# Kernel tuning notes

Measured on AMD Instinct MI355X. Metric: run time of the kernel, lower is better.

Reference implementation:

```python
import jax, jax.numpy as jnp
import numpy as np

N_NODES = 100000
N_EDGES = 1600000
DIMS = [2, 16, 32, 32, 32, 32, 32, 16, 2]


def setup_inputs() -> dict:
    key = jax.random.key(0)
    ks = jax.random.split(key, 20)
    inp = {}
    inp["x"] = jax.random.normal(ks[0], (N_NODES, DIMS[0]), dtype=jnp.float32)
    inp["edge_index"] = jax.random.randint(ks[1], (2, N_EDGES), 0, N_NODES, dtype=jnp.int64)
    for i in range(8):
        fan_in, fan_out = DIMS[i], DIMS[i + 1]
        scale = 1.0 / np.sqrt(fan_in)
        inp[f"W{i+1}"] = jax.random.uniform(ks[2 + i], (fan_in, fan_out), minval=-scale, maxval=scale, dtype=jnp.float32)
        inp[f"b{i+1}"] = jnp.zeros((fan_out,), dtype=jnp.float32)
    return inp


def _gcn_layer(h, W, b, src, dst, norm, n):
    # GCNConv: h' = D^{-1/2} (A+I) D^{-1/2} (h W) + b
    m = (h @ W)[src] * norm[:, None]          # [E+N, d_out] gathered messages
    return jax.ops.segment_sum(m, dst, num_segments=n) + b


def reference(x, edge_index, W1, b1, W2, b2, W3, b3, W4, b4, W5, b5, W6, b6, W7, b7, W8, b8):
    n = x.shape[0]
    x_orig = x[:, :2]
    loops = jnp.arange(n, dtype=edge_index.dtype)
    src = jnp.concatenate([edge_index[0], loops])  # self-loops appended
    dst = jnp.concatenate([edge_index[1], loops])
    deg = jax.ops.segment_sum(jnp.ones(src.shape[0], x.dtype), dst, num_segments=n)
    dinv = jnp.where(deg > 0, jax.lax.rsqrt(deg), 0.0)
    norm = dinv[src] * dinv[dst]               # symmetric normalization per edge
    params = [(W1, b1), (W2, b2), (W3, b3), (W4, b4), (W5, b5), (W6, b6), (W7, b7), (W8, b8)]
    h = x
    for i, (W, b) in enumerate(params):
        h = _gcn_layer(h, W, b, src, dst, norm, n)
        if i < 7:
            h = jax.nn.relu(h)  # dropout is identity in eval mode
    return h + x_orig
```

## Files before the change

### kernel.cpp

```cpp
#include <hip/hip_runtime.h>
#include <hip/hip_fp16.h>

#define NN 100000
#define NE 1600000
#define SCAN_BLK 1024
#define NBLK ((NN + SCAN_BLK - 1) / SCAN_BLK)

#define EB 3072
#define NBE ((NE + EB - 1) / EB)
#define BSH 10
#define NBUCK ((NN + 1023) >> BSH)
#define BCAP 18432


__global__ void k_init(int* __restrict__ bcur) {
    int i = blockIdx.x * blockDim.x + threadIdx.x;
    if (i < NBUCK) bcur[i] = i * BCAP;
}

__global__ __launch_bounds__(256) void k_bucket(
    const int* __restrict__ ei, int* __restrict__ bcur,
    long long* __restrict__ pairs, int nE) {
    __shared__ int cnt[NBUCK];
    __shared__ int sc[NBUCK];
    __shared__ int rc[NBUCK];
    __shared__ int gbase[NBUCK];
    __shared__ int tmp[256];
    __shared__ long long st[EB];

    int base = blockIdx.x * EB;
    int lim = nE - base; if (lim > EB) lim = EB;
    int tid = threadIdx.x;

    for (int i = tid; i < NBUCK; i += 256) cnt[i] = 0;
    __syncthreads();
    for (int i = tid; i < lim; i += 256) {
        int d = ei[nE + base + i];
        atomicAdd(&cnt[d >> BSH], 1);
    }
    __syncthreads();
    {
        int v = (tid < NBUCK) ? cnt[tid] : 0;
        tmp[tid] = v;
        __syncthreads();
        for (int off = 1; off < 256; off <<= 1) {
            int add = (tid >= off) ? tmp[tid - off] : 0;
            __syncthreads();
            tmp[tid] += add;
            __syncthreads();
        }
        if (tid < NBUCK) {
            int e = tmp[tid] - v;
            sc[tid] = e;
            rc[tid] = e;
            gbase[tid] = (v > 0) ? atomicAdd(&bcur[tid], v) : 0;
        }
    }
    __syncthreads();
    for (int i = tid; i < lim; i += 256) {
        int s = ei[base + i];
        int d = ei[nE + base + i];
        int p = atomicAdd(&rc[d >> BSH], 1);
        st[p] = ((long long)d << 32) | (unsigned int)s;
    }
    __syncthreads();
    for (int i = tid; i < lim; i += 256) {
        long long pr = st[i];
        int b = (int)(pr >> 32) >> BSH;
        pairs[gbase[b] + (i - sc[b])] = pr;
    }
}

__global__ __launch_bounds__(256) void k_count2(
    const long long* __restrict__ pairs, const int* __restrict__ bcur,
    int* __restrict__ deg) {
    __shared__ int cnt[1 << BSH];
    int b = blockIdx.x;
    int gb = b * BCAP;
    int m = bcur[b] - gb;
    for (int i = threadIdx.x; i < (1 << BSH); i += 256) cnt[i] = 0;
    __syncthreads();
    for (int i = threadIdx.x; i < m; i += 256) {
        int d = (int)(pairs[gb + i] >> 32);
        atomicAdd(&cnt[d & ((1 << BSH) - 1)], 1);
    }
    __syncthreads();
    int base = b << BSH;
    for (int i = threadIdx.x; i < (1 << BSH); i += 256) {
        int v = base + i;
        if (v < NN) deg[v] = cnt[i];
    }
}

__global__ __launch_bounds__(SCAN_BLK) void k_scan1(
    const int* __restrict__ deg, int* __restrict__ exc, int* __restrict__ bsum, int n) {
    __shared__ int sh[SCAN_BLK];
    int tid = threadIdx.x;
    int i = blockIdx.x * SCAN_BLK + tid;
    int v = (i < n) ? ((deg[i] + 7) & ~7) : 0;
    sh[tid] = v;
    __syncthreads();
    for (int off = 1; off < SCAN_BLK; off <<= 1) {
        int add = (tid >= off) ? sh[tid - off] : 0;
        __syncthreads();
        sh[tid] += add;
        __syncthreads();
    }
    if (i < n) exc[i] = sh[tid] - v;
    if (tid == SCAN_BLK - 1) bsum[blockIdx.x] = sh[tid];
}

__global__ __launch_bounds__(128) void k_scan2(int* __restrict__ bsum, int nb) {
    __shared__ int sh[128];
    int tid = threadIdx.x;
    int v = (tid < nb) ? bsum[tid] : 0;
    sh[tid] = v;
    __syncthreads();
    for (int off = 1; off < 128; off <<= 1) {
        int add = (tid >= off) ? sh[tid - off] : 0;
        __syncthreads();
        sh[tid] += add;
        __syncthreads();
    }
    if (tid < nb) bsum[tid] = sh[tid] - v;
}

__global__ __launch_bounds__(SCAN_BLK) void k_scan3(
    const int* __restrict__ exc, const int* __restrict__ bsum,
    const int* __restrict__ deg, const float* __restrict__ x,
    int* __restrict__ rowptr, float* __restrict__ dinv,
    __half2* __restrict__ hd0, int n) {
    int i = blockIdx.x * SCAN_BLK + threadIdx.x;
    if (i >= n) return;
    int r = exc[i] + bsum[blockIdx.x];
    rowptr[i] = r;
    float dv = rsqrtf((float)(deg[i] + 1));
    dinv[i] = dv;
    hd0[i] = __floats2half2_rn(x[2 * i] * dv, x[2 * i + 1] * dv);
    if (i == n - 1) rowptr[n] = r + ((deg[i] + 7) & ~7);
    if (i == 0) hd0[n] = __floats2half2_rn(0.f, 0.f);
}

__global__ __launch_bounds__(256) void k_fill3(
    const long long* __restrict__ pairs, const int* __restrict__ bcur,
    const int* __restrict__ rowptr, int* __restrict__ csr_src) {
    __shared__ int lcur[1 << BSH];
    int b = blockIdx.x;
    int gb = b * BCAP;
    int m = bcur[b] - gb;
    int base = b << BSH;
    for (int i = threadIdx.x; i < (1 << BSH); i += 256) {
        int v = base + i;
        lcur[i] = (v < NN) ? rowptr[v] : 0;
    }
    __syncthreads();
    for (int i = threadIdx.x; i < m; i += 256) {
        long long pr = pairs[gb + i];
        int d = (int)(pr >> 32);
        int s = (int)(pr & 0xffffffffLL);
        int pos = atomicAdd(&lcur[d & ((1 << BSH) - 1)], 1);
        csr_src[pos] = s;
    }
    __syncthreads();
    for (int i = threadIdx.x; i < (1 << BSH); i += 256) {
        int v = base + i;
        if (v < NN) {
            int e = lcur[i];
            int pe = rowptr[v + 1];
            for (; e < pe; ++e) csr_src[e] = NN;
        }
    }
}


__global__ __launch_bounds__(256) void k_layer1(
    const int* __restrict__ rowptr, const int* __restrict__ csr_src,
    const __half2* __restrict__ hd0, const float* __restrict__ Wg,
    const float* __restrict__ bg, const float* __restrict__ dinv,
    __half* __restrict__ hd1, int n) {
    __shared__ float sW[32];
    if (threadIdx.x < 32) sW[threadIdx.x] = Wg[threadIdx.x];
    __syncthreads();
    int v = blockIdx.x * 16 + threadIdx.x / 16;
    int l = threadIdx.x & 15;
    if (v > n) return;
    if (v == n) { hd1[v * 16 + l] = __float2half(0.f); return; }
    int lo = rowptr[v], hi = rowptr[v + 1];
    float a0 = 0.f, a1 = 0.f;
    for (int j = lo + l; j < hi; j += 16) {
        float2 h = __half22float2(hd0[csr_src[j]]);
        a0 += h.x; a1 += h.y;
    }
#pragma unroll
    for (int off = 8; off >= 1; off >>= 1) {
        a0 += __shfl_xor(a0, off, 16);
        a1 += __shfl_xor(a1, off, 16);
    }
    float dv = dinv[v];
    float2 hs = __half22float2(hd0[v]);
    a0 = (a0 + hs.x) * dv;
    a1 = (a1 + hs.y) * dv;
    float o = bg[l] + a0 * sW[l] + a1 * sW[16 + l];
    hd1[v * 16 + l] = __float2half(fmaxf(o, 0.f) * dv);
}

template <int DIN, int DOUT, bool RELU, bool LAST, bool TWOWAY>
__global__ __launch_bounds__(256) void k_layer(
    const int* __restrict__ rowptr, const int* __restrict__ csr_src,
    const __half* __restrict__ hd_in, const float* __restrict__ Wg,
    const float* __restrict__ bg, const float* __restrict__ dinv,
    const float* __restrict__ xorig, __half* __restrict__ hout_h,
    float* __restrict__ hout_f, int n) {
    constexpr int OPL = (DOUT + DIN - 1) / DIN;
    constexpr int LPG = DIN * (TWOWAY ? 2 : 1);
    __shared__ float sW[DIN * DOUT];
    for (int i = threadIdx.x; i < DIN * DOUT; i += 256) sW[i] = Wg[i];
    __syncthreads();
    const int gpb = 256 / LPG;
    int v = blockIdx.x * gpb + (int)threadIdx.x / LPG;
    int f = threadIdx.x % DIN;
    int way = (threadIdx.x % LPG) / DIN;
    if (v > n) return;
    if (v == n) {
        if (!LAST && way == 0) {
#pragma unroll
            for (int k = 0; k < OPL; ++k) {
                int g = f + k * DIN;
                if (g < DOUT) hout_h[v * DOUT + g] = __float2half(0.f);
            }
        }
        return;
    }
    int lo = rowptr[v], hi = rowptr[v + 1];
    if (TWOWAY) {
        int nch = (hi - lo) >> 3;
        int mid = lo + (((nch + 1) >> 1) << 3);
        if (way == 0) hi = mid; else lo = mid;
    }
    float acc = 0.f;
    for (int j = lo; j < hi; j += 8) {
        int s0 = csr_src[j + 0], s1 = csr_src[j + 1], s2 = csr_src[j + 2], s3 = csr_src[j + 3];
        int s4 = csr_src[j + 4], s5 = csr_src[j + 5], s6 = csr_src[j + 6], s7 = csr_src[j + 7];
        float v0 = __half2float(hd_in[s0 * DIN + f]);
        float v1 = __half2float(hd_in[s1 * DIN + f]);
        float v2 = __half2float(hd_in[s2 * DIN + f]);
        float v3 = __half2float(hd_in[s3 * DIN + f]);
        float v4 = __half2float(hd_in[s4 * DIN + f]);
        float v5 = __half2float(hd_in[s5 * DIN + f]);
        float v6 = __half2float(hd_in[s6 * DIN + f]);
        float v7 = __half2float(hd_in[s7 * DIN + f]);
        acc += ((v0 + v1) + (v2 + v3)) + ((v4 + v5) + (v6 + v7));
    }
    if (TWOWAY) acc += __shfl_xor(acc, DIN, 64);
    float dv = dinv[v];
    float aggv = (acc + __half2float(hd_in[v * DIN + f])) * dv;

    if (TWOWAY) {
        int g = f % DOUT;
        float o = (way == 0) ? bg[g] : 0.f;
        int f2b = way * (DIN / 2);
#pragma unroll
        for (int k = 0; k < DIN / 2; ++k) {
            int f2 = f2b + k;
            o = fmaf(__shfl(aggv, f2, DIN), sW[f2 * DOUT + g], o);
        }
        o += __shfl_xor(o, DIN, 64);
        if (way == 0 && f < DOUT) {
            float r = o;
            if (RELU) r = fmaxf(r, 0.f);
            if (LAST) hout_f[v * DOUT + g] = r + xorig[v * 2 + g];
            else      hout_h[v * DOUT + g] = __float2half(r * dv);
        }
    } else {
        float o[OPL];
#pragma unroll
        for (int k = 0; k < OPL; ++k) {
            int g = f + k * DIN;
            o[k] = (g < DOUT) ? bg[g] : 0.f;
        }
#pragma unroll
        for (int f2 = 0; f2 < DIN; ++f2) {
            float hf = __shfl(aggv, f2, DIN);
#pragma unroll
            for (int k = 0; k < OPL; ++k) {
                int g = f + k * DIN;
                if (g < DOUT) o[k] = fmaf(hf, sW[f2 * DOUT + g], o[k]);
            }
        }
#pragma unroll
        for (int k = 0; k < OPL; ++k) {
            int g = f + k * DIN;
            if (g < DOUT) {
                float r = o[k];
                if (RELU) r = fmaxf(r, 0.f);
                if (LAST) hout_f[v * DOUT + g] = r + xorig[v * 2 + g];
                else      hout_h[v * DOUT + g] = __float2half(r * dv);
            }
        }
    }
}


extern "C" void kernel_launch(void* const* d_in, const int* in_sizes, int n_in,
                              void* d_out, int out_size, void* d_ws, size_t ws_size,
                              hipStream_t stream) {
    const float* x = (const float*)d_in[0];
    const int* ei = (const int*)d_in[1];
    const float* W[8];
    const float* B[8];
    for (int i = 0; i < 8; ++i) {
        W[i] = (const float*)d_in[2 + 2 * i];
        B[i] = (const float*)d_in[3 + 2 * i];
    }
    float* out = (float*)d_out;

    char* ws = (char*)d_ws;
    int*       deg     = (int*)      (ws + 0);
    float*     dinv    = (float*)    (ws + 400128);
    int*       rowptr  = (int*)      (ws + 800256);
    int*       exc     = (int*)      (ws + 1200384);
    int*       bsum    = (int*)      (ws + 1600512);
    int*       bcur    = (int*)      (ws + 1601024);
    long long* pairs   = (long long*)(ws + 1601536);
    int*       csr_src = (int*)      (ws + 16052224);
    __half*    hdA     = (__half*)   (ws + 25652224);
    __half*    hdB     = (__half*)   (ws + 32052352);

    dim3 blk(256);

    k_init<<<1, 128, 0, stream>>>(bcur);
    k_bucket<<<NBE, blk, 0, stream>>>(ei, bcur, pairs, NE);
    k_count2<<<NBUCK, blk, 0, stream>>>(pairs, bcur, deg);
    k_scan1<<<NBLK, SCAN_BLK, 0, stream>>>(deg, exc, bsum, NN);
    k_scan2<<<1, 128, 0, stream>>>(bsum, NBLK);
    k_scan3<<<NBLK, SCAN_BLK, 0, stream>>>(exc, bsum, deg, x, rowptr, dinv, (__half2*)hdA, NN);
    k_fill3<<<NBUCK, blk, 0, stream>>>(pairs, bcur, rowptr, csr_src);

    int g16 = (NN + 16) / 16;
    int gT  = (NN + 4) / 4;

    k_layer1<<<g16, blk, 0, stream>>>(rowptr, csr_src, (const __half2*)hdA, W[0], B[0], dinv, hdB, NN);
    k_layer<16, 32, true, false, false><<<g16, blk, 0, stream>>>(rowptr, csr_src, hdB, W[1], B[1], dinv, x, hdA, out, NN);
    k_layer<32, 32, true, false, true><<<gT, blk, 0, stream>>>(rowptr, csr_src, hdA, W[2], B[2], dinv, x, hdB, out, NN);
    k_layer<32, 32, true, false, true><<<gT, blk, 0, stream>>>(rowptr, csr_src, hdB, W[3], B[3], dinv, x, hdA, out, NN);
    k_layer<32, 32, true, false, true><<<gT, blk, 0, stream>>>(rowptr, csr_src, hdA, W[4], B[4], dinv, x, hdB, out, NN);
    k_layer<32, 32, true, false, true><<<gT, blk, 0, stream>>>(rowptr, csr_src, hdB, W[5], B[5], dinv, x, hdA, out, NN);
    k_layer<32, 16, true, false, true><<<gT, blk, 0, stream>>>(rowptr, csr_src, hdA, W[6], B[6], dinv, x, hdB, out, NN);
    k_layer<16, 2, false, true, false><<<g16, blk, 0, stream>>>(rowptr, csr_src, hdB, W[7], B[7], dinv, x, hdA, out, NN);
}
```

Baseline: 395.1 us.

## Map one node per wavefront with scalar neighbor indices in GCN layers

Rewrites the per-layer aggregation kernel so that each 64-lane wavefront processes a single node. The rowptr bounds and neighbor indices become wave-uniform via readfirstlane, so they can be loaded through scalar loads. Each layer shape gets its own specialized mini-matmul that splits the input features across lanes and reduces with shuffles. The intent is to cut redundant vector index loads and per-lane address math. In exchange, lanes are wasted for narrow layers (DIN=16, each gathered feature read by multiple lanes) and parallelism per node is lower. The edge-bucketing block size is also doubled.

New measurement: 448.0 us. 1.13x slower.

```diff
diff --git a/kernel.cpp b/kernel.cpp
--- a/kernel.cpp
+++ b/kernel.cpp
@@ -6,7 +6,7 @@
 #define SCAN_BLK 1024
 #define NBLK ((NN + SCAN_BLK - 1) / SCAN_BLK)
 
-#define EB 3072
+#define EB 6144
 #define NBE ((NE + EB - 1) / EB)
 #define BSH 10
 #define NBUCK ((NN + 1023) >> BSH)
@@ -204,99 +204,93 @@
     hd1[v * 16 + l] = __float2half(fmaxf(o, 0.f) * dv);
 }
 
-template <int DIN, int DOUT, bool RELU, bool LAST, bool TWOWAY>
-__global__ __launch_bounds__(256) void k_layer(
+template <int DIN, int DOUT, bool RELU, bool LAST>
+__global__ __launch_bounds__(256) void k_layerS(
     const int* __restrict__ rowptr, const int* __restrict__ csr_src,
     const __half* __restrict__ hd_in, const float* __restrict__ Wg,
     const float* __restrict__ bg, const float* __restrict__ dinv,
     const float* __restrict__ xorig, __half* __restrict__ hout_h,
     float* __restrict__ hout_f, int n) {
-    constexpr int OPL = (DOUT + DIN - 1) / DIN;
-    constexpr int LPG = DIN * (TWOWAY ? 2 : 1);
     __shared__ float sW[DIN * DOUT];
     for (int i = threadIdx.x; i < DIN * DOUT; i += 256) sW[i] = Wg[i];
     __syncthreads();
-    const int gpb = 256 / LPG;
-    int v = blockIdx.x * gpb + (int)threadIdx.x / LPG;
-    int f = threadIdx.x % DIN;
-    int way = (threadIdx.x % LPG) / DIN;
-    if (v > n) return;
-    if (v == n) {
-        if (!LAST && way == 0) {
-#pragma unroll
-            for (int k = 0; k < OPL; ++k) {
-                int g = f + k * DIN;
-                if (g < DOUT) hout_h[v * DOUT + g] = __float2half(0.f);
-            }
-        }
+    int lane = threadIdx.x & 63;
+    int vu = __builtin_amdgcn_readfirstlane(blockIdx.x * 4 + (threadIdx.x >> 6));
+    if (vu > n) return;
+    int f = lane & (DIN - 1);
+    if (vu == n) {
+        if (!LAST && lane < DOUT) hout_h[(size_t)vu * DOUT + lane] = __float2half(0.f);
         return;
     }
-    int lo = rowptr[v], hi = rowptr[v + 1];
-    if (TWOWAY) {
-        int nch = (hi - lo) >> 3;
-        int mid = lo + (((nch + 1) >> 1) << 3);
-        if (way == 0) hi = mid; else lo = mid;
-    }
+    int lo = __builtin_amdgcn_readfirstlane(rowptr[vu]);
+    int hi = __builtin_amdgcn_readfirstlane(rowptr[vu + 1]);
     float acc = 0.f;
     for (int j = lo; j < hi; j += 8) {
-        int s0 = csr_src[j + 0], s1 = csr_src[j + 1], s2 = csr_src[j + 2], s3 = csr_src[j + 3];
-        int s4 = csr_src[j + 4], s5 = csr_src[j + 5], s6 = csr_src[j + 6], s7 = csr_src[j + 7];
-        float v0 = __half2float(hd_in[s0 * DIN + f]);
-        float v1 = __half2float(hd_in[s1 * DIN + f]);
-        float v2 = __half2float(hd_in[s2 * DIN + f]);
-        float v3 = __half2float(hd_in[s3 * DIN + f]);
-        float v4 = __half2float(hd_in[s4 * DIN + f]);
-        float v5 = __half2float(hd_in[s5 * DIN + f]);
-        float v6 = __half2float(hd_in[s6 * DIN + f]);
-        float v7 = __half2float(hd_in[s7 * DIN + f]);
-        acc += ((v0 + v1) + (v2 + v3)) + ((v4 + v5) + (v6 + v7));
-    }
-    if (TWOWAY) acc += __shfl_xor(acc, DIN, 64);
-    float dv = dinv[v];
-    float aggv = (acc + __half2float(hd_in[v * DIN + f])) * dv;
-
-    if (TWOWAY) {
-        int g = f % DOUT;
-        float o = (way == 0) ? bg[g] : 0.f;
-        int f2b = way * (DIN / 2);
-#pragma unroll
-        for (int k = 0; k < DIN / 2; ++k) {
+#pragma unroll
+        for (int k = 0; k < 8; ++k) {
+            int s = __builtin_amdgcn_readfirstlane(csr_src[j + k]);
+            acc += __half2float(hd_in[(size_t)s * DIN + f]);
+        }
+    }
+    float dv = dinv[vu];
+    float aggv = (acc + __half2float(hd_in[(size_t)vu * DIN + f])) * dv;
+
+    float o = 0.f;
+    if constexpr (DIN == 32 && DOUT == 32) {
+        int g = lane & 31;
+        int f2b = (lane >> 5) << 4;
+#pragma unroll
+        for (int k = 0; k < 16; ++k) {
             int f2 = f2b + k;
-            o = fmaf(__shfl(aggv, f2, DIN), sW[f2 * DOUT + g], o);
-        }
-        o += __shfl_xor(o, DIN, 64);
-        if (way == 0 && f < DOUT) {
-            float r = o;
-            if (RELU) r = fmaxf(r, 0.f);
-            if (LAST) hout_f[v * DOUT + g] = r + xorig[v * 2 + g];
-            else      hout_h[v * DOUT + g] = __float2half(r * dv);
+            o = fmaf(__shfl(aggv, f2, 32), sW[f2 * 32 + g], o);
+        }
+        o += __shfl_xor(o, 32, 64);
+        o += bg[g];
+        if (lane < 32) {
+            if (RELU) o = fmaxf(o, 0.f);
+            hout_h[(size_t)vu * 32 + g] = __float2half(o * dv);
+        }
+    } else if constexpr (DIN == 32 && DOUT == 16) {
+        int g = lane & 15;
+        int q = lane >> 4;
+#pragma unroll
+        for (int k = 0; k < 8; ++k) {
+            int f2 = q * 8 + k;
+            o = fmaf(__shfl(aggv, f2, 32), sW[f2 * 16 + g], o);
+        }
+        o += __shfl_xor(o, 16, 64);
+        o += __shfl_xor(o, 32, 64);
+        o += bg[g];
+        if (lane < 16) {
+            if (RELU) o = fmaxf(o, 0.f);
+            hout_h[(size_t)vu * 16 + g] = __float2half(o * dv);
+        }
+    } else if constexpr (DIN == 16 && DOUT == 32) {
+        int g = lane & 31;
+        int h = lane >> 5;
+#pragma unroll
+        for (int k = 0; k < 8; ++k) {
+            int f2 = h * 8 + k;
+            o = fmaf(__shfl(aggv, f2, 16), sW[f2 * 32 + g], o);
+        }
+        o += __shfl_xor(o, 32, 64);
+        o += bg[g];
+        if (lane < 32) {
+            if (RELU) o = fmaxf(o, 0.f);
+            hout_h[(size_t)vu * 32 + g] = __float2half(o * dv);
         }
     } else {
-        float o[OPL];
-#pragma unroll
-        for (int k = 0; k < OPL; ++k) {
-            int g = f + k * DIN;
-            o[k] = (g < DOUT) ? bg[g] : 0.f;
-        }
-#pragma unroll
-        for (int f2 = 0; f2 < DIN; ++f2) {
-            float hf = __shfl(aggv, f2, DIN);
-#pragma unroll
-            for (int k = 0; k < OPL; ++k) {
-                int g = f + k * DIN;
-                if (g < DOUT) o[k] = fmaf(hf, sW[f2 * DOUT + g], o[k]);
-            }
-        }
-#pragma unroll
-        for (int k = 0; k < OPL; ++k) {
-            int g = f + k * DIN;
-            if (g < DOUT) {
-                float r = o[k];
-                if (RELU) r = fmaxf(r, 0.f);
-                if (LAST) hout_f[v * DOUT + g] = r + xorig[v * 2 + g];
-                else      hout_h[v * DOUT + g] = __float2half(r * dv);
-            }
-        }
+        int g = lane & 1;
+        int rep = lane >> 4;
+#pragma unroll
+        for (int k = 0; k < 4; ++k) {
+            int f2 = rep * 4 + k;
+            o = fmaf(__shfl(aggv, f2, 16), sW[f2 * 2 + g], o);
+        }
+        o += __shfl_xor(o, 16, 64);
+        o += __shfl_xor(o, 32, 64);
+        o += bg[g];
+        if (lane < 2) hout_f[(size_t)vu * 2 + g] = o + xorig[(size_t)vu * 2 + g];
     }
 }
 
@@ -336,15 +330,16 @@
     k_scan3<<<NBLK, SCAN_BLK, 0, stream>>>(exc, bsum, deg, x, rowptr, dinv, (__half2*)hdA, NN);
     k_fill3<<<NBUCK, blk, 0, stream>>>(pairs, bcur, rowptr, csr_src);
 
-    int g16 = (NN + 16) / 16;
-    int gT  = (NN + 4) / 4;
-
-    k_layer1<<<g16, blk, 0, stream>>>(rowptr, csr_src, (const __half2*)hdA, W[0], B[0], dinv, hdB, NN);
-    k_layer<16, 32, true, false, false><<<g16, blk, 0, stream>>>(rowptr, csr_src, hdB, W[1], B[1], dinv, x, hdA, out, NN);
-    k_layer<32, 32, true, false, true><<<gT, blk, 0, stream>>>(rowptr, csr_src, hdA, W[2], B[2], dinv, x, hdB, out, NN);
-    k_layer<32, 32, true, false, true><<<gT, blk, 0, stream>>>(rowptr, csr_src, hdB, W[3], B[3], dinv, x, hdA, out, NN);
-    k_layer<32, 32, true, false, true><<<gT, blk, 0, stream>>>(rowptr, csr_src, hdA, W[4], B[4], dinv, x, hdB, out, NN);
-    k_layer<32, 32, true, false, true><<<gT, blk, 0, stream>>>(rowptr, csr_src, hdB, W[5], B[5], dinv, x, hdA, out, NN);
-    k_layer<32, 16, true, false, true><<<gT, blk, 0, stream>>>(rowptr, csr_src, hdA, W[6], B[6], dinv, x, hdB, out, NN);
-    k_layer<16, 2, false, true, false><<<g16, blk, 0, stream>>>(rowptr, csr_src, hdB, W[7], B[7], dinv, x, hdA, out, NN);
-}
+    int g1 = (NN + 16) / 16;
+    int gS = NN / 4 + 1;
+    int gL = (NN + 3) / 4;
+
+    k_layer1<<<g1, blk, 0, stream>>>(rowptr, csr_src, (const __half2*)hdA, W[0], B[0], dinv, hdB, NN);
+    k_layerS<16, 32, true, false><<<gS, blk, 0, stream>>>(rowptr, csr_src, hdB, W[1], B[1], dinv, x, hdA, out, NN);
+    k_layerS<32, 32, true, false><<<gS, blk, 0, stream>>>(rowptr, csr_src, hdA, W[2], B[2], dinv, x, hdB, out, NN);
+    k_layerS<32, 32, true, false><<<gS, blk, 0, stream>>>(rowptr, csr_src, hdB, W[3], B[3], dinv, x, hdA, out, NN);
+    k_layerS<32, 32, true, false><<<gS, blk, 0, stream>>>(rowptr, csr_src, hdA, W[4], B[4], dinv, x, hdB, out, NN);
+    k_layerS<32, 32, true, false><<<gS, blk, 0, stream>>>(rowptr, csr_src, hdB, W[5], B[5], dinv, x, hdA, out, NN);
+    k_layerS<32, 16, true, false><<<gS, blk, 0, stream>>>(rowptr, csr_src, hdA, W[6], B[6], dinv, x, hdB, out, NN);
+    k_layerS<16, 2, false, true><<<gL, blk, 0, stream>>>(rowptr, csr_src, hdB, W[7], B[7], dinv, x, hdA, out, NN);
+}
```
